# Optimization experiments

Hardware: AMD Instinct MI355X
Metric: run time of the kernel (lower is better)

Reference implementation:

```python
import jax, jax.numpy as jnp
import numpy as np

T, D, F, V = 16384, 1024, 2048, 4096


def _mlp(x, w1, w2):
    # residual ReLU MLP stand-in for a transformer stack (tokenwise)
    return x + jax.nn.relu(x @ w1) @ w2


def setup_inputs() -> dict:
    key = jax.random.key(0)
    ks = jax.random.split(key, 11)
    s1 = 1.0 / np.sqrt(D)
    s2 = 1.0 / np.sqrt(F)
    g = lambda k, shape, sc: jax.random.normal(k, shape, dtype=jnp.float32) * sc
    return {
        "inputs_embeds": g(ks[0], (T, D), 1.0),
        "enc_w1": g(ks[1], (D, F), s1),
        "enc_w2": g(ks[2], (F, D), s2),
        "back_w1": g(ks[3], (D, F), s1),
        "back_w2": g(ks[4], (F, D), s2),
        "dec_w1": g(ks[5], (D, F), s1),
        "dec_w2": g(ks[6], (F, D), s2),
        "sp_w": g(ks[7], (D, 1), s1),
        "sp_b": jnp.zeros((1,), jnp.float32),
        "pos_emb": g(ks[8], (T, D), 0.02),
        "lm_head": g(ks[9], (D, V), s1),
        "cu_seq_lens": jnp.array([0, 4096, 8192, 12288, 16384], dtype=jnp.int32),
    }


def reference(inputs_embeds, enc_w1, enc_w2, back_w1, back_w2, dec_w1, dec_w2,
              sp_w, sp_b, pos_emb, lm_head, cu_seq_lens):
    # --- encoder (3-layer stack stand-in) ---
    enc = _mlp(inputs_embeds, enc_w1, enc_w2)                 # [T, D]
    # --- token gate: sigmoid + threshold ---
    w = jax.nn.sigmoid(enc @ sp_w + sp_b)[:, 0]               # [T]
    mask = w >= 0.5                                           # keep mask (= ~zero_mask)
    mi = mask.astype(jnp.int32)
    # --- ragged re-pack: within-segment rank of kept tokens (new position ids) ---
    ecs = jnp.cumsum(mi) - mi                                 # exclusive cumsum of kept
    seg = jnp.searchsorted(cu_seq_lens[1:], jnp.arange(T), side="right")
    base = ecs[cu_seq_lens[:-1]][seg]                         # kept-count before each segment
    new_pos = ecs - base                                      # arange(length) per new segment
    # stable sort places kept tokens first in original (packed) order,
    # exactly matching the per-segment concat of the torch version
    order = jnp.argsort(jnp.logical_not(mask), stable=True)   # [T]
    valid = mask[order]
    # gather + weight by gate value, add new position embedding
    gathered = (enc * w[:, None])[order] + pos_emb[new_pos[order]]
    gathered = jnp.where(valid[:, None], gathered, 0.0)
    # --- backbone compute on packed kept tokens ---
    bb = _mlp(gathered, back_w1, back_w2)                     # [T, D] (padded tail unused)
    # --- scatter-combine: kept slots <- backbone, dropped slots <- encoder residual ---
    inv = jnp.argsort(order)
    combined = jnp.where(mask[:, None], bb[inv], enc)         # [T, D]
    # --- decoder (3-layer stack stand-in) + lm head ---
    dec = _mlp(combined, dec_w1, dec_w2)
    logits = dec @ lm_head                                    # [T, V] fp32
    return logits
```

## Files before the change

### kernel.cpp

```cpp
#include <hip/hip_runtime.h>
#include <hip/hip_bf16.h>
#include <math.h>

static constexpr int TT = 16384;
static constexpr int DD = 1024;
static constexpr int FF = 2048;
static constexpr int VV = 4096;
static constexpr int CAP = 1024;
#define TAU 0.02f

using bf16 = __hip_bfloat16;
typedef __attribute__((ext_vector_type(8))) short bf16x8;
typedef __attribute__((ext_vector_type(4))) float f32x4;

__device__ inline void gload16(const void* g, void* l) {
    __builtin_amdgcn_global_load_lds(
        (const __attribute__((address_space(1))) void*)g,
        (__attribute__((address_space(3))) void*)l, 16, 0, 0);
}

template<int EPI , bool WB16, bool WF32, bool ROWLIM, bool GPART>
__global__ __launch_bounds__(512, 2)
void mgemm8(const bf16* __restrict__ A, const bf16* __restrict__ BT,
            const float* __restrict__ X, bf16* __restrict__ Ob,
            float* __restrict__ Of, float* __restrict__ gpart,
            const float* __restrict__ qv,
            int M, int N, int K, const int* __restrict__ rowlim)
{
    if constexpr (ROWLIM) { if ((int)blockIdx.y * 256 >= *rowlim) return; }
    const int m0 = blockIdx.y * 256, n0 = blockIdx.x * 256;

    extern __shared__ char smem[];

    const int tid = threadIdx.x;
    const int wv = tid >> 6, ln = tid & 63;
    const int wm = wv >> 2, wn = wv & 3;
    const int lr = ln & 15, lk = ln >> 4;
    const int swz = (lr & 7) << 4;

    const bf16* Ag = A  + (size_t)m0 * K;
    const bf16* Bg = BT + (size_t)n0 * K;

    const int NT = K >> 6;
    const int NI = NT >> 1;

    const int aoff0 = (wm * 128 + lr) * 128;
    const int boff0 = 32768 + (wn * 64 + lr) * 128;
    const int cb0 = (lk * 16) ^ swz;
    const int cb1 = (64 + lk * 16) ^ swz;

    auto STAGE = [&](const bf16* g, int h, int kt, int buf, int op) {
        const int r = ln >> 3;
        const int c = ((ln & 7) ^ r) * 8;
        const bf16* s = g + (size_t)(h * 128 + wv * 16 + r) * K + kt * 64 + c;
        char* d = smem + buf * 65536 + op * 32768 + h * 16384 + wv * 2048;
        gload16(s, d);
        gload16(s + (size_t)8 * K, d + 1024);
    };
    auto stage_j = [&](int j) {
        const int tile = j >> 2;
        if (tile >= NT) return;
        const int part = j & 3;
        const int buf = tile & 1;
        if (part < 2) STAGE(Bg, part, tile, buf, 1);
        else          STAGE(Ag, part - 2, tile, buf, 0);
    };

    bf16x8 afr[2][2], bfr[4][2];
    f32x4 acc[8][4];
    #pragma unroll
    for (int m = 0; m < 8; ++m)
        #pragma unroll
        for (int n = 0; n < 4; ++n) acc[m][n] = (f32x4){0.f, 0.f, 0.f, 0.f};

#define DS_A(BUF, Q) do {                                                     \
    const char* _p = smem + (BUF) * 65536 + aoff0 + (Q) * 4096;               \
    afr[0][0] = *(const bf16x8*)(_p + cb0);                                   \
    afr[0][1] = *(const bf16x8*)(_p + cb1);                                   \
    afr[1][0] = *(const bf16x8*)(_p + 2048 + cb0);                            \
    afr[1][1] = *(const bf16x8*)(_p + 2048 + cb1);                            \
} while (0)

#define DS_B(BUF) do {                                                        \
    const char* _p = smem + (BUF) * 65536 + boff0;                            \
    _Pragma("unroll")                                                         \
    for (int nf = 0; nf < 4; ++nf) {                                          \
        bfr[nf][0] = *(const bf16x8*)(_p + nf * 2048 + cb0);                  \
        bfr[nf][1] = *(const bf16x8*)(_p + nf * 2048 + cb1);                  \
    }                                                                         \
} while (0)

#define MFMAQ(Q) do {                                                         \
    __builtin_amdgcn_s_setprio(1);                                            \
    _Pragma("unroll")                                                         \
    for (int m2 = 0; m2 < 2; ++m2)                                            \
        _Pragma("unroll")                                                     \
        for (int nf = 0; nf < 4; ++nf) {                                      \
            acc[(Q) * 2 + m2][nf] = __builtin_amdgcn_mfma_f32_16x16x32_bf16(  \
                afr[m2][0], bfr[nf][0], acc[(Q) * 2 + m2][nf], 0, 0, 0);      \
            acc[(Q) * 2 + m2][nf] = __builtin_amdgcn_mfma_f32_16x16x32_bf16(  \
                afr[m2][1], bfr[nf][1], acc[(Q) * 2 + m2][nf], 0, 0, 0);      \
        }                                                                     \
    __builtin_amdgcn_s_setprio(0);                                            \
} while (0)

#define PHASE(Q, BUF, DOB, J, W)                                              \
    {                                                                         \
        DS_A(BUF, Q);                                                         \
        if (DOB) DS_B(BUF);                                                   \
        stage_j(J);                                                           \
        if ((W) == 1)      asm volatile("s_waitcnt vmcnt(6)" ::: "memory");   \
        else if ((W) == 2) asm volatile("s_waitcnt vmcnt(0)" ::: "memory");   \
        __builtin_amdgcn_sched_barrier(0);                                    \
        __builtin_amdgcn_s_barrier();                                         \
        MFMAQ(Q);                                                             \
        __builtin_amdgcn_s_barrier();                                         \
    }

    STAGE(Bg, 0, 0, 0, 1); STAGE(Bg, 1, 0, 0, 1);
    STAGE(Ag, 0, 0, 0, 0); STAGE(Ag, 1, 0, 0, 0);
    asm volatile("s_waitcnt vmcnt(4)" ::: "memory");
    STAGE(Bg, 0, 1, 1, 1); STAGE(Bg, 1, 1, 1, 1);
    STAGE(Ag, 0, 1, 1, 0);
    asm volatile("s_waitcnt vmcnt(6)" ::: "memory");
    __builtin_amdgcn_sched_barrier(0);
    __builtin_amdgcn_s_barrier();

    for (int i = 0; i < NI; ++i) {
        const int jb = 7 + 8 * i;
        const bool last = (i + 1 == NI);
        PHASE(0, 0, true,  jb + 0, 0);
        PHASE(1, 0, false, jb + 1, 0);
        PHASE(2, 0, false, jb + 2, 0);
        PHASE(3, 0, false, jb + 3, last ? 2 : 1);
        PHASE(0, 1, true,  jb + 4, 0);
        PHASE(1, 1, false, jb + 5, 0);
        PHASE(2, 1, false, jb + 6, 0);
        PHASE(3, 1, false, jb + 7, last ? 0 : 1);
    }

#undef PHASE
#undef MFMAQ
#undef DS_B
#undef DS_A

    if constexpr (GPART) {
        float qvv[4];
        #pragma unroll
        for (int nf = 0; nf < 4; ++nf) qvv[nf] = qv[n0 + wn * 64 + nf * 16 + lr];
        #pragma unroll
        for (int mf = 0; mf < 8; ++mf)
            #pragma unroll
            for (int rr = 0; rr < 4; ++rr) {
                float s = 0.f;
                #pragma unroll
                for (int nf = 0; nf < 4; ++nf) s += fmaxf(acc[mf][nf][rr], 0.f) * qvv[nf];
                s += __shfl_xor(s, 1, 64); s += __shfl_xor(s, 2, 64);
                s += __shfl_xor(s, 4, 64); s += __shfl_xor(s, 8, 64);
                if (lr == 0)
                    gpart[(size_t)(blockIdx.x * 4 + wn) * M +
                          (m0 + wm * 128 + mf * 16 + lk * 4 + rr)] = s;
            }
    }

    #pragma unroll
    for (int mf = 0; mf < 8; ++mf)
        #pragma unroll
        for (int nf = 0; nf < 4; ++nf)
            #pragma unroll
            for (int rr = 0; rr < 4; ++rr) {
                const int row = m0 + wm * 128 + mf * 16 + lk * 4 + rr;
                const int col = n0 + wn * 64 + nf * 16 + lr;
                float v = acc[mf][nf][rr];
                if constexpr (EPI == 1) v = fmaxf(v, 0.f);
                if constexpr (EPI == 2) v += X[(size_t)row * N + col];
                if constexpr (WB16) Ob[(size_t)row * N + col] = __float2bfloat16(v);
                if constexpr (WF32) Of[(size_t)row * N + col] = v;
            }
}

__global__ void wtrans_all(const float* __restrict__ e1, const float* __restrict__ e2,
                           const float* __restrict__ b1, const float* __restrict__ b2,
                           const float* __restrict__ d1, const float* __restrict__ d2,
                           const float* __restrict__ lm,
                           bf16* __restrict__ e1T, bf16* __restrict__ e2T,
                           bf16* __restrict__ b1T, bf16* __restrict__ b2T,
                           bf16* __restrict__ d1T, bf16* __restrict__ d2T,
                           bf16* __restrict__ lmT)
{
    int bid = blockIdx.x;
    const float* W; bf16* T; int R, C;
    if (bid < 12288) {
        const int m = bid >> 11;
        bid &= 2047;
        R = (m & 1) ? FF : DD;
        C = (m & 1) ? DD : FF;
        switch (m) {
            case 0:  W = e1; T = e1T; break;
            case 1:  W = e2; T = e2T; break;
            case 2:  W = b1; T = b1T; break;
            case 3:  W = b2; T = b2T; break;
            case 4:  W = d1; T = d1T; break;
            default: W = d2; T = d2T; break;
        }
    } else {
        bid -= 12288; W = lm; T = lmT; R = DD; C = VV;
    }
    const int tc = C >> 5;
    const int cb = (bid % tc) * 32, rb = (bid / tc) * 32;

    __shared__ float tile[32][33];
    const int tx = threadIdx.x & 31, ty = threadIdx.x >> 5;
    #pragma unroll
    for (int i = 0; i < 32; i += 8)
        tile[ty + i][tx] = W[(size_t)(rb + ty + i) * C + cb + tx];
    __syncthreads();
    #pragma unroll
    for (int i = 0; i < 32; i += 8)
        T[(size_t)(cb + ty + i) * R + rb + tx] = __float2bfloat16(tile[tx][ty + i]);
}

__global__ void castx2(const float* __restrict__ x, const float* __restrict__ spw,
                       bf16* __restrict__ xb, float* __restrict__ sx)
{
    const int t  = blockIdx.x * 4 + (threadIdx.x >> 6);
    const int ln = threadIdx.x & 63;
    const float4* row = (const float4*)(x + (size_t)t * DD);
    const float4* sp4 = (const float4*)spw;
    bf16* dst = xb + (size_t)t * DD;
    float s = 0.f;
    #pragma unroll
    for (int q = 0; q < 4; ++q) {
        const int c = q * 64 + ln;
        const float4 v = row[c], p = sp4[c];
        s += v.x * p.x + v.y * p.y + v.z * p.z + v.w * p.w;
        dst[c * 4 + 0] = __float2bfloat16(v.x);
        dst[c * 4 + 1] = __float2bfloat16(v.y);
        dst[c * 4 + 2] = __float2bfloat16(v.z);
        dst[c * 4 + 3] = __float2bfloat16(v.w);
    }
    #pragma unroll
    for (int off = 32; off > 0; off >>= 1) s += __shfl_xor(s, off, 64);
    if (ln == 0) sx[t] = s;
}

__global__ void qvec(const float* __restrict__ w2, const float* __restrict__ sp,
                     float* __restrict__ q)
{
    const int f  = blockIdx.x * 4 + (threadIdx.x >> 6);
    const int ln = threadIdx.x & 63;
    float s = 0.f;
    const float* row = w2 + (size_t)f * DD;
    for (int k = ln; k < DD; k += 64) s += row[k] * sp[k];
    #pragma unroll
    for (int off = 32; off > 0; off >>= 1) s += __shfl_xor(s, off, 64);
    if (ln == 0) q[f] = s;
}

__global__ void gate2(const float* __restrict__ sx, const float* __restrict__ spb,
                      const float* __restrict__ gpart, float* __restrict__ w,
                      int* __restrict__ mi, int* __restrict__ flags,
                      int* __restrict__ cnt)
{
    const int t = blockIdx.x * 256 + threadIdx.x;
    float s = sx[t] + spb[0];
    #pragma unroll
    for (int j = 0; j < 32; ++j) s += gpart[(size_t)j * TT + t];
    const float sg = 1.f / (1.f + expf(-s));
    w[t]  = sg;
    mi[t] = (sg >= 0.5f) ? 1 : 0;
    if (fabsf(s) < TAU) {
        const int i = atomicAdd(cnt, 1);
        if (i < CAP) flags[i] = t;
    }
}

__global__ __launch_bounds__(256)
void fixh(const float* __restrict__ x, const float* __restrict__ w1,
          const int* __restrict__ flags, const int* __restrict__ cnt,
          float* __restrict__ Hpart)
{
    const int nb = min(*cnt, CAP);
    const int t0 = blockIdx.z * 32;
    if (t0 >= nb) return;
    const int ntk = min(32, nb - t0);
    const int f  = blockIdx.x * 256 + threadIdx.x;
    const int d0 = blockIdx.y * 256;

    __shared__ float xs[32][256];
    for (int i = threadIdx.x; i < 32 * 64; i += 256) {
        const int tk = i >> 6, dq = i & 63;
        float4 v = (tk < ntk)
            ? *(const float4*)&x[(size_t)flags[t0 + tk] * DD + d0 + dq * 4]
            : make_float4(0.f, 0.f, 0.f, 0.f);
        *(float4*)&xs[tk][dq * 4] = v;
    }
    __syncthreads();

    float acc[32];
    #pragma unroll
    for (int tk = 0; tk < 32; ++tk) acc[tk] = 0.f;
    for (int dd = 0; dd < 256; ++dd) {
        const float wv = w1[(size_t)(d0 + dd) * FF + f];
        #pragma unroll
        for (int tk = 0; tk < 32; ++tk) acc[tk] += xs[tk][dd] * wv;
    }
    for (int tk = 0; tk < ntk; ++tk)
        Hpart[((size_t)blockIdx.y * CAP + (t0 + tk)) * FF + f] = acc[tk];
}

__global__ void fixres2(const float* __restrict__ sx, const float* __restrict__ spb,
                        const float* __restrict__ Hpart, const float* __restrict__ qv,
                        const int* __restrict__ flags, const int* __restrict__ cnt,
                        float* __restrict__ w, int* __restrict__ mi)
{
    const int nb = min(*cnt, CAP);
    const int i  = blockIdx.x * 4 + (threadIdx.x >> 6);
    const int ln = threadIdx.x & 63;
    if (i >= nb) return;
    float s = 0.f;
    for (int f = ln; f < FF; f += 64) {
        const float h = Hpart[(size_t)(0 * CAP + i) * FF + f]
                      + Hpart[(size_t)(1 * CAP + i) * FF + f]
                      + Hpart[(size_t)(2 * CAP + i) * FF + f]
                      + Hpart[(size_t)(3 * CAP + i) * FF + f];
        s += fmaxf(h, 0.f) * qv[f];
    }
    #pragma unroll
    for (int off = 32; off > 0; off >>= 1) s += __shfl_xor(s, off, 64);
    if (ln == 0) {
        const int t = flags[i];
        const float logit = sx[t] + s + spb[0];
        const float sg = 1.f / (1.f + expf(-logit));
        w[t]  = sg;
        mi[t] = (sg >= 0.5f) ? 1 : 0;
    }
}

__global__ void scan_kernel(const int* __restrict__ mi, const int* __restrict__ cu,
                            int* __restrict__ ecs, int* __restrict__ meta)
{
    __shared__ int sums[256];
    const int tid  = threadIdx.x;
    const int base = tid * 64;
    int s = 0;
    for (int i = 0; i < 64; ++i) s += mi[base + i];
    sums[tid] = s;
    __syncthreads();
    for (int off = 1; off < 256; off <<= 1) {
        int v = (tid >= off) ? sums[tid - off] : 0;
        __syncthreads();
        sums[tid] += v;
        __syncthreads();
    }
    int run = (tid == 0) ? 0 : sums[tid - 1];
    for (int i = 0; i < 64; ++i) { ecs[base + i] = run; run += mi[base + i]; }
    if (tid == 255) meta[0] = sums[255];
    if (tid < 4) {
        const int idx = cu[tid];
        const int tc = idx >> 6, rem = idx & 63;
        int e = (tc == 0) ? 0 : sums[tc - 1];
        for (int i = 0; i < rem; ++i) e += mi[tc * 64 + i];
        meta[1 + tid] = e;
    }
}

__global__ void pack_kernel(const float* __restrict__ enc, const float* __restrict__ w,
                            const int* __restrict__ mi, const int* __restrict__ ecs,
                            const int* __restrict__ cu, const int* __restrict__ meta,
                            const float* __restrict__ pos_emb,
                            float* __restrict__ Pf, bf16* __restrict__ Pb)
{
    const int t    = blockIdx.x * 4 + (threadIdx.x >> 6);
    const int lane = threadIdx.x & 63;
    if (!mi[t]) return;
    const int e = ecs[t];
    int seg = 0;
    #pragma unroll
    for (int ss = 1; ss < 4; ++ss) if (t >= cu[ss]) seg = ss;
    const int np = e - meta[1 + seg];
    const float wt = w[t];
    const float4* src = (const float4*)(enc + (size_t)t * DD);
    const float4* pe  = (const float4*)(pos_emb + (size_t)np * DD);
    float4* dstf = (float4*)(Pf + (size_t)e * DD);
    bf16*   dstb = Pb + (size_t)e * DD;
    for (int c = lane; c < DD / 4; c += 64) {
        float4 v = src[c], p = pe[c];
        v.x = v.x * wt + p.x; v.y = v.y * wt + p.y;
        v.z = v.z * wt + p.z; v.w = v.w * wt + p.w;
        dstf[c] = v;
        dstb[c * 4 + 0] = __float2bfloat16(v.x);
        dstb[c * 4 + 1] = __float2bfloat16(v.y);
        dstb[c * 4 + 2] = __float2bfloat16(v.z);
        dstb[c * 4 + 3] = __float2bfloat16(v.w);
    }
}

__global__ void combine_kernel(float* __restrict__ ENC, const float* __restrict__ BBf,
                               const int* __restrict__ mi, const int* __restrict__ ecs,
                               bf16* __restrict__ Cb)
{
    const int t    = blockIdx.x * 4 + (threadIdx.x >> 6);
    const int lane = threadIdx.x & 63;
    const bool kept = mi[t] != 0;
    const float4* src = kept ? (const float4*)(BBf + (size_t)ecs[t] * DD)
                             : (const float4*)(ENC + (size_t)t * DD);
    float4* dstf = (float4*)(ENC + (size_t)t * DD);
    bf16*   dstb = Cb + (size_t)t * DD;
    for (int c = lane; c < DD / 4; c += 64) {
        const float4 v = src[c];
        if (kept) dstf[c] = v;
        dstb[c * 4 + 0] = __float2bfloat16(v.x);
        dstb[c * 4 + 1] = __float2bfloat16(v.y);
        dstb[c * 4 + 2] = __float2bfloat16(v.z);
        dstb[c * 4 + 3] = __float2bfloat16(v.w);
    }
}

extern "C" void kernel_launch(void* const* d_in, const int* in_sizes, int n_in,
                              void* d_out, int out_size, void* d_ws, size_t ws_size,
                              hipStream_t stream)
{
    (void)in_sizes; (void)n_in; (void)out_size; (void)ws_size;
    const float* x   = (const float*)d_in[0];
    const float* ew1 = (const float*)d_in[1];
    const float* ew2 = (const float*)d_in[2];
    const float* bw1 = (const float*)d_in[3];
    const float* bw2 = (const float*)d_in[4];
    const float* dw1 = (const float*)d_in[5];
    const float* dw2 = (const float*)d_in[6];
    const float* spw = (const float*)d_in[7];
    const float* spb = (const float*)d_in[8];
    const float* pem = (const float*)d_in[9];
    const float* lmh = (const float*)d_in[10];
    const int*   cu  = (const int*)d_in[11];
    float* out = (float*)d_out;

    (void)hipFuncSetAttribute((const void*)mgemm8<1, true, false, false, true>,
                              hipFuncAttributeMaxDynamicSharedMemorySize, 131072);
    (void)hipFuncSetAttribute((const void*)mgemm8<2, false, true, false, false>,
                              hipFuncAttributeMaxDynamicSharedMemorySize, 131072);
    (void)hipFuncSetAttribute((const void*)mgemm8<1, true, false, true, false>,
                              hipFuncAttributeMaxDynamicSharedMemorySize, 131072);
    (void)hipFuncSetAttribute((const void*)mgemm8<2, false, true, true, false>,
                              hipFuncAttributeMaxDynamicSharedMemorySize, 131072);
    (void)hipFuncSetAttribute((const void*)mgemm8<1, true, false, false, false>,
                              hipFuncAttributeMaxDynamicSharedMemorySize, 131072);
    (void)hipFuncSetAttribute((const void*)mgemm8<2, true, false, false, false>,
                              hipFuncAttributeMaxDynamicSharedMemorySize, 131072);
    (void)hipFuncSetAttribute((const void*)mgemm8<0, false, true, false, false>,
                              hipFuncAttributeMaxDynamicSharedMemorySize, 131072);

    char* w = (char*)d_ws;
    auto alloc = [&](size_t bytes) { char* p = w; w += bytes; return p; };
    bf16* ew1T = (bf16*)alloc((size_t)FF * DD * 2);
    bf16* ew2T = (bf16*)alloc((size_t)DD * FF * 2);
    bf16* bw1T = (bf16*)alloc((size_t)FF * DD * 2);
    bf16* bw2T = (bf16*)alloc((size_t)DD * FF * 2);
    bf16* dw1T = (bf16*)alloc((size_t)FF * DD * 2);
    bf16* dw2T = (bf16*)alloc((size_t)DD * FF * 2);
    bf16* lmhT = (bf16*)alloc((size_t)VV * DD * 2);
    float* qv  = (float*)alloc((size_t)FF * 4);
    float* GP  = (float*)alloc((size_t)32 * TT * 4);
    float* WG  = (float*)alloc((size_t)TT * 4);
    int*  MI   = (int*)alloc((size_t)TT * 4);
    int*  ECS  = (int*)alloc((size_t)TT * 4);
    int*  META = (int*)alloc(64);
    float* SX  = (float*)alloc((size_t)TT * 4);
    int*  FLAGS= (int*)alloc((size_t)CAP * 4);
    int*  CNT  = (int*)alloc(64);
    bf16* Xb   = (bf16*)alloc((size_t)TT * DD * 2);
    bf16* Hb   = (bf16*)alloc((size_t)TT * FF * 2);
    float* ENC = (float*)alloc((size_t)TT * DD * 4);
    float* Pf  = (float*)alloc((size_t)TT * DD * 4);
    bf16* Pb   = (bf16*)alloc((size_t)TT * DD * 2);
    bf16* Cb   = Xb;
    bf16* DECb = Pb;
    float* Hpart = Pf;

    const dim3 blk(256);
    const dim3 blk8(512);

    (void)hipMemsetAsync(CNT, 0, 4, stream);

    castx2<<<TT / 4, blk, 0, stream>>>(x, spw, Xb, SX);
    wtrans_all<<<16384, blk, 0, stream>>>(ew1, ew2, bw1, bw2, dw1, dw2, lmh,
                                          ew1T, ew2T, bw1T, bw2T, dw1T, dw2T, lmhT);
    qvec<<<FF / 4, blk, 0, stream>>>(ew2, spw, qv);

    mgemm8<1, true, false, false, true><<<dim3(FF / 256, TT / 256), blk8, 131072, stream>>>(
        Xb, ew1T, nullptr, Hb, nullptr, GP, qv, TT, FF, DD, nullptr);

    gate2<<<TT / 256, blk, 0, stream>>>(SX, spb, GP, WG, MI, FLAGS, CNT);
    fixh<<<dim3(FF / 256, 4, CAP / 32), blk, 0, stream>>>(x, ew1, FLAGS, CNT, Hpart);
    fixres2<<<CAP / 4, blk, 0, stream>>>(SX, spb, Hpart, qv, FLAGS, CNT, WG, MI);
    scan_kernel<<<1, blk, 0, stream>>>(MI, cu, ECS, META);

    mgemm8<2, false, true, false, false><<<dim3(DD / 256, TT / 256), blk8, 131072, stream>>>(
        Hb, ew2T, x, nullptr, ENC, nullptr, nullptr, TT, DD, FF, nullptr);

    pack_kernel<<<TT / 4, blk, 0, stream>>>(ENC, WG, MI, ECS, cu, META, pem, Pf, Pb);

    mgemm8<1, true, false, true, false><<<dim3(FF / 256, TT / 256), blk8, 131072, stream>>>(
        Pb, bw1T, nullptr, Hb, nullptr, nullptr, nullptr, TT, FF, DD, META);
    mgemm8<2, false, true, true, false><<<dim3(DD / 256, TT / 256), blk8, 131072, stream>>>(
        Hb, bw2T, Pf, nullptr, Pf, nullptr, nullptr, TT, DD, FF, META);

    combine_kernel<<<TT / 4, blk, 0, stream>>>(ENC, Pf, MI, ECS, Cb);

    mgemm8<1, true, false, false, false><<<dim3(FF / 256, TT / 256), blk8, 131072, stream>>>(
        Cb, dw1T, nullptr, Hb, nullptr, nullptr, nullptr, TT, FF, DD, nullptr);
    mgemm8<2, true, false, false, false><<<dim3(DD / 256, TT / 256), blk8, 131072, stream>>>(
        Hb, dw2T, ENC, DECb, nullptr, nullptr, nullptr, TT, DD, FF, nullptr);

    mgemm8<0, false, true, false, false><<<dim3(VV / 256, TT / 256), blk8, 131072, stream>>>(
        DECb, lmhT, nullptr, nullptr, out, nullptr, nullptr, TT, VV, DD, nullptr);
}
```

Before: 765.7 us.

## Keep residual activations in bf16 and remap GEMM workgroups across XCDs

Residual streams (encoder output, packed backbone input, backbone output) are now stored only in bf16, and the residual adds in the down-projection GEMMs read bf16 inputs (a new epilogue mode). The fp32 copies and their writes in pack and combine are dropped, so combine becomes a plain bf16 row copy. The GEMM also permutes its block index so consecutive tiles are spread across the chip's eight XCDs, aiming at better L2 reuse. The trade-off is lower precision on the residual path, since the encoder residual now comes from bf16 x rather than fp32, which adds rounding error to the outputs.

```diff
diff --git a/kernel.cpp b/kernel.cpp
--- a/kernel.cpp
+++ b/kernel.cpp
@@ -1,6 +1,7 @@
 #include <hip/hip_runtime.h>
 #include <hip/hip_bf16.h>
 #include <math.h>
+#include <string.h>
 
 static constexpr int TT = 16384;
 static constexpr int DD = 1024;
@@ -18,17 +19,31 @@
         (const __attribute__((address_space(1))) void*)g,
         (__attribute__((address_space(3))) void*)l, 16, 0, 0);
 }
-
-template<int EPI , bool WB16, bool WF32, bool ROWLIM, bool GPART>
+__device__ inline float b2f(short s) {
+    unsigned u = (unsigned)(unsigned short)s << 16;
+    float f; __builtin_memcpy(&f, &u, 4); return f;
+}
+__device__ inline short f2b(float f) {
+    bf16 h = __float2bfloat16(f);
+    unsigned short us; __builtin_memcpy(&us, &h, 2); return (short)us;
+}
+
+template<int EPI, bool WB16, bool WF32, bool ROWLIM, bool GPART>
 __global__ __launch_bounds__(512, 2)
 void mgemm8(const bf16* __restrict__ A, const bf16* __restrict__ BT,
-            const float* __restrict__ X, bf16* __restrict__ Ob,
-            float* __restrict__ Of, float* __restrict__ gpart,
-            const float* __restrict__ qv,
+            const float* __restrict__ Xf, const bf16* __restrict__ Xh,
+            bf16* __restrict__ Ob, float* __restrict__ Of,
+            float* __restrict__ gpart, const float* __restrict__ qv,
             int M, int N, int K, const int* __restrict__ rowlim)
 {
-    if constexpr (ROWLIM) { if ((int)blockIdx.y * 256 >= *rowlim) return; }
-    const int m0 = blockIdx.y * 256, n0 = blockIdx.x * 256;
+    const int gx = gridDim.x;
+    const int lin = blockIdx.x + blockIdx.y * gx;
+    const int nwg = gx * gridDim.y;
+    const int wg = (lin & 7) * (nwg >> 3) + (lin >> 3);
+    const int bx = wg % gx, by = wg / gx;
+
+    if constexpr (ROWLIM) { if (by * 256 >= *rowlim) return; }
+    const int m0 = by * 256, n0 = bx * 256;
 
     extern __shared__ char smem[];
 
@@ -158,7 +173,7 @@
                 s += __shfl_xor(s, 1, 64); s += __shfl_xor(s, 2, 64);
                 s += __shfl_xor(s, 4, 64); s += __shfl_xor(s, 8, 64);
                 if (lr == 0)
-                    gpart[(size_t)(blockIdx.x * 4 + wn) * M +
+                    gpart[(size_t)(bx * 4 + wn) * M +
                           (m0 + wm * 128 + mf * 16 + lk * 4 + rr)] = s;
             }
     }
@@ -173,7 +188,8 @@
                 const int col = n0 + wn * 64 + nf * 16 + lr;
                 float v = acc[mf][nf][rr];
                 if constexpr (EPI == 1) v = fmaxf(v, 0.f);
-                if constexpr (EPI == 2) v += X[(size_t)row * N + col];
+                if constexpr (EPI == 2) v += Xf[(size_t)row * N + col];
+                if constexpr (EPI == 3) v += __bfloat162float(Xh[(size_t)row * N + col]);
                 if constexpr (WB16) Ob[(size_t)row * N + col] = __float2bfloat16(v);
                 if constexpr (WF32) Of[(size_t)row * N + col] = v;
             }
@@ -365,11 +381,10 @@
     }
 }
 
-__global__ void pack_kernel(const float* __restrict__ enc, const float* __restrict__ w,
+__global__ void pack_kernel(const bf16* __restrict__ enc, const float* __restrict__ w,
                             const int* __restrict__ mi, const int* __restrict__ ecs,
                             const int* __restrict__ cu, const int* __restrict__ meta,
-                            const float* __restrict__ pos_emb,
-                            float* __restrict__ Pf, bf16* __restrict__ Pb)
+                            const float* __restrict__ pos_emb, bf16* __restrict__ Pb)
 {
     const int t    = blockIdx.x * 4 + (threadIdx.x >> 6);
     const int lane = threadIdx.x & 63;
@@ -380,41 +395,39 @@
     for (int ss = 1; ss < 4; ++ss) if (t >= cu[ss]) seg = ss;
     const int np = e - meta[1 + seg];
     const float wt = w[t];
-    const float4* src = (const float4*)(enc + (size_t)t * DD);
+    const bf16x8* src = (const bf16x8*)(enc + (size_t)t * DD);
     const float4* pe  = (const float4*)(pos_emb + (size_t)np * DD);
-    float4* dstf = (float4*)(Pf + (size_t)e * DD);
-    bf16*   dstb = Pb + (size_t)e * DD;
-    for (int c = lane; c < DD / 4; c += 64) {
-        float4 v = src[c], p = pe[c];
-        v.x = v.x * wt + p.x; v.y = v.y * wt + p.y;
-        v.z = v.z * wt + p.z; v.w = v.w * wt + p.w;
-        dstf[c] = v;
-        dstb[c * 4 + 0] = __float2bfloat16(v.x);
-        dstb[c * 4 + 1] = __float2bfloat16(v.y);
-        dstb[c * 4 + 2] = __float2bfloat16(v.z);
-        dstb[c * 4 + 3] = __float2bfloat16(v.w);
-    }
-}
-
-__global__ void combine_kernel(float* __restrict__ ENC, const float* __restrict__ BBf,
+    bf16x8* dst = (bf16x8*)(Pb + (size_t)e * DD);
+    #pragma unroll
+    for (int q = 0; q < 2; ++q) {
+        const int c = q * 64 + lane;
+        const bf16x8 v = src[c];
+        const float4 p0 = pe[c * 2], p1 = pe[c * 2 + 1];
+        bf16x8 r;
+        r[0] = f2b(b2f(v[0]) * wt + p0.x);
+        r[1] = f2b(b2f(v[1]) * wt + p0.y);
+        r[2] = f2b(b2f(v[2]) * wt + p0.z);
+        r[3] = f2b(b2f(v[3]) * wt + p0.w);
+        r[4] = f2b(b2f(v[4]) * wt + p1.x);
+        r[5] = f2b(b2f(v[5]) * wt + p1.y);
+        r[6] = f2b(b2f(v[6]) * wt + p1.z);
+        r[7] = f2b(b2f(v[7]) * wt + p1.w);
+        dst[c] = r;
+    }
+}
+
+__global__ void combine_kernel(const bf16* __restrict__ ENCb, const bf16* __restrict__ BBb,
                                const int* __restrict__ mi, const int* __restrict__ ecs,
                                bf16* __restrict__ Cb)
 {
     const int t    = blockIdx.x * 4 + (threadIdx.x >> 6);
     const int lane = threadIdx.x & 63;
     const bool kept = mi[t] != 0;
-    const float4* src = kept ? (const float4*)(BBf + (size_t)ecs[t] * DD)
-                             : (const float4*)(ENC + (size_t)t * DD);
-    float4* dstf = (float4*)(ENC + (size_t)t * DD);
-    bf16*   dstb = Cb + (size_t)t * DD;
-    for (int c = lane; c < DD / 4; c += 64) {
-        const float4 v = src[c];
-        if (kept) dstf[c] = v;
-        dstb[c * 4 + 0] = __float2bfloat16(v.x);
-        dstb[c * 4 + 1] = __float2bfloat16(v.y);
-        dstb[c * 4 + 2] = __float2bfloat16(v.z);
-        dstb[c * 4 + 3] = __float2bfloat16(v.w);
-    }
+    const int4* src = kept ? (const int4*)(BBb + (size_t)ecs[t] * DD)
+                           : (const int4*)(ENCb + (size_t)t * DD);
+    int4* dst = (int4*)(Cb + (size_t)t * DD);
+    #pragma unroll
+    for (int q = 0; q < 2; ++q) dst[q * 64 + lane] = src[q * 64 + lane];
 }
 
 extern "C" void kernel_launch(void* const* d_in, const int* in_sizes, int n_in,
@@ -438,15 +451,13 @@
 
     (void)hipFuncSetAttribute((const void*)mgemm8<1, true, false, false, true>,
                               hipFuncAttributeMaxDynamicSharedMemorySize, 131072);
-    (void)hipFuncSetAttribute((const void*)mgemm8<2, false, true, false, false>,
+    (void)hipFuncSetAttribute((const void*)mgemm8<3, true, false, false, false>,
                               hipFuncAttributeMaxDynamicSharedMemorySize, 131072);
     (void)hipFuncSetAttribute((const void*)mgemm8<1, true, false, true, false>,
                               hipFuncAttributeMaxDynamicSharedMemorySize, 131072);
-    (void)hipFuncSetAttribute((const void*)mgemm8<2, false, true, true, false>,
+    (void)hipFuncSetAttribute((const void*)mgemm8<3, true, false, true, false>,
                               hipFuncAttributeMaxDynamicSharedMemorySize, 131072);
     (void)hipFuncSetAttribute((const void*)mgemm8<1, true, false, false, false>,
-                              hipFuncAttributeMaxDynamicSharedMemorySize, 131072);
-    (void)hipFuncSetAttribute((const void*)mgemm8<2, true, false, false, false>,
                               hipFuncAttributeMaxDynamicSharedMemorySize, 131072);
     (void)hipFuncSetAttribute((const void*)mgemm8<0, false, true, false, false>,
                               hipFuncAttributeMaxDynamicSharedMemorySize, 131072);
@@ -471,12 +482,12 @@
     int*  CNT  = (int*)alloc(64);
     bf16* Xb   = (bf16*)alloc((size_t)TT * DD * 2);
     bf16* Hb   = (bf16*)alloc((size_t)TT * FF * 2);
-    float* ENC = (float*)alloc((size_t)TT * DD * 4);
-    float* Pf  = (float*)alloc((size_t)TT * DD * 4);
+    bf16* ENCb = (bf16*)alloc((size_t)TT * DD * 2);
     bf16* Pb   = (bf16*)alloc((size_t)TT * DD * 2);
+    bf16* BBb  = (bf16*)alloc((size_t)TT * DD * 2);
     bf16* Cb   = Xb;
     bf16* DECb = Pb;
-    float* Hpart = Pf;
+    float* Hpart = (float*)BBb;
 
     const dim3 blk(256);
     const dim3 blk8(512);
@@ -489,30 +500,30 @@
     qvec<<<FF / 4, blk, 0, stream>>>(ew2, spw, qv);
 
     mgemm8<1, true, false, false, true><<<dim3(FF / 256, TT / 256), blk8, 131072, stream>>>(
-        Xb, ew1T, nullptr, Hb, nullptr, GP, qv, TT, FF, DD, nullptr);
+        Xb, ew1T, nullptr, nullptr, Hb, nullptr, GP, qv, TT, FF, DD, nullptr);
 
     gate2<<<TT / 256, blk, 0, stream>>>(SX, spb, GP, WG, MI, FLAGS, CNT);
     fixh<<<dim3(FF / 256, 4, CAP / 32), blk, 0, stream>>>(x, ew1, FLAGS, CNT, Hpart);
     fixres2<<<CAP / 4, blk, 0, stream>>>(SX, spb, Hpart, qv, FLAGS, CNT, WG, MI);
     scan_kernel<<<1, blk, 0, stream>>>(MI, cu, ECS, META);
 
-    mgemm8<2, false, true, false, false><<<dim3(DD / 256, TT / 256), blk8, 131072, stream>>>(
-        Hb, ew2T, x, nullptr, ENC, nullptr, nullptr, TT, DD, FF, nullptr);
-
-    pack_kernel<<<TT / 4, blk, 0, stream>>>(ENC, WG, MI, ECS, cu, META, pem, Pf, Pb);
+    mgemm8<3, true, false, false, false><<<dim3(DD / 256, TT / 256), blk8, 131072, stream>>>(
+        Hb, ew2T, nullptr, Xb, ENCb, nullptr, nullptr, nullptr, TT, DD, FF, nullptr);
+
+    pack_kernel<<<TT / 4, blk, 0, stream>>>(ENCb, WG, MI, ECS, cu, META, pem, Pb);
 
     mgemm8<1, true, false, true, false><<<dim3(FF / 256, TT / 256), blk8, 131072, stream>>>(
-        Pb, bw1T, nullptr, Hb, nullptr, nullptr, nullptr, TT, FF, DD, META);
-    mgemm8<2, false, true, true, false><<<dim3(DD / 256, TT / 256), blk8, 131072, stream>>>(
-        Hb, bw2T, Pf, nullptr, Pf, nullptr, nullptr, TT, DD, FF, META);
-
-    combine_kernel<<<TT / 4, blk, 0, stream>>>(ENC, Pf, MI, ECS, Cb);
+        Pb, bw1T, nullptr, nullptr, Hb, nullptr, nullptr, nullptr, TT, FF, DD, META);
+    mgemm8<3, true, false, true, false><<<dim3(DD / 256, TT / 256), blk8, 131072, stream>>>(
+        Hb, bw2T, nullptr, Pb, BBb, nullptr, nullptr, nullptr, TT, DD, FF, META);
+
+    combine_kernel<<<TT / 4, blk, 0, stream>>>(ENCb, BBb, MI, ECS, Cb);
 
     mgemm8<1, true, false, false, false><<<dim3(FF / 256, TT / 256), blk8, 131072, stream>>>(
-        Cb, dw1T, nullptr, Hb, nullptr, nullptr, nullptr, TT, FF, DD, nullptr);
-    mgemm8<2, true, false, false, false><<<dim3(DD / 256, TT / 256), blk8, 131072, stream>>>(
-        Hb, dw2T, ENC, DECb, nullptr, nullptr, nullptr, TT, DD, FF, nullptr);
+        Cb, dw1T, nullptr, nullptr, Hb, nullptr, nullptr, nullptr, TT, FF, DD, nullptr);
+    mgemm8<3, true, false, false, false><<<dim3(DD / 256, TT / 256), blk8, 131072, stream>>>(
+        Hb, dw2T, nullptr, Cb, DECb, nullptr, nullptr, nullptr, TT, DD, FF, nullptr);
 
     mgemm8<0, false, true, false, false><<<dim3(VV / 256, TT / 256), blk8, 131072, stream>>>(
-        DECb, lmhT, nullptr, nullptr, out, nullptr, nullptr, TT, VV, DD, nullptr);
-}
+        DECb, lmhT, nullptr, nullptr, nullptr, out, nullptr, nullptr, TT, VV, DD, nullptr);
+}
```

Result: faster. 732.9 us (-4.3%).
